# Performance work log

Measured on AMD Instinct MI355X. Metric: run time of the kernel, lower is better.

The kernel has to match this reference:

```python
import jax, jax.numpy as jnp
import numpy as np

D = 192      # d_model
DE = 96      # d_edge
H = 8        # n_heads
DH = D // H  # d_head = 24
DF = 2 * D   # ff hidden = 384
N = 25000
E = 400000


def _layernorm(x, s, b, eps=1e-5):
    m = jnp.mean(x, axis=-1, keepdims=True)
    v = jnp.var(x, axis=-1, keepdims=True)
    return (x - m) * jax.lax.rsqrt(v + eps) * s + b


def setup_inputs() -> dict:
    key = jax.random.key(0)
    ks = jax.random.split(key, 12)
    sc = lambda d: 1.0 / np.sqrt(d)
    inp = {
        "x": jax.random.normal(ks[0], (N, D), jnp.float32),
        "edge_feat": jax.random.normal(ks[1], (E, DE), jnp.float32),
        "edge_index": jax.random.randint(ks[2], (2, E), 0, N, jnp.int64),
        # attention projections (stored [d_in, d_out], applied as x @ W)
        "Wq": jax.random.normal(ks[3], (D, D), jnp.float32) * sc(D),
        "Wk": jax.random.normal(ks[4], (D, D), jnp.float32) * sc(D),
        "Wv": jax.random.normal(ks[5], (D, D), jnp.float32) * sc(D),
        "We": jax.random.normal(ks[6], (DE, H), jnp.float32) * sc(DE),
        "Wo": jax.random.normal(ks[7], (D, D), jnp.float32) * sc(D),
        "bo": jnp.zeros((D,), jnp.float32),
        "Wg": jax.random.normal(ks[8], (2 * D, D), jnp.float32) * sc(2 * D),
        "bg": jnp.zeros((D,), jnp.float32),
        "ln1_s": jnp.ones((D,), jnp.float32),
        "ln1_b": jnp.zeros((D,), jnp.float32),
        "Wf1": jax.random.normal(ks[9], (D, DF), jnp.float32) * sc(D),
        "bf1": jnp.zeros((DF,), jnp.float32),
        "Wf2": jax.random.normal(ks[10], (DF, D), jnp.float32) * sc(DF),
        "bf2": jnp.zeros((D,), jnp.float32),
        "ln2_s": jnp.ones((D,), jnp.float32),
        "ln2_b": jnp.zeros((D,), jnp.float32),
    }
    return inp


def reference(x, edge_feat, edge_index, Wq, Wk, Wv, We, Wo, bo, Wg, bg,
              ln1_s, ln1_b, Wf1, bf1, Wf2, bf2, ln2_s, ln2_b):
    src, dst = edge_index[0], edge_index[1]
    n = x.shape[0]
    # per-edge gathered projections: [E, H, DH]
    q = (x[dst] @ Wq).reshape(-1, H, DH)
    k = (x[src] @ Wk).reshape(-1, H, DH)
    v = (x[src] @ Wv).reshape(-1, H, DH)
    score = jnp.sum(q * k, axis=-1) / np.sqrt(DH) + edge_feat @ We  # [E, H]
    # segment softmax over incoming edges of each dst node
    mx = jax.ops.segment_max(score, dst, num_segments=n)           # [N, H]
    alpha = jnp.exp(score - mx[dst])                                # [E, H]
    den = jax.ops.segment_sum(alpha, dst, num_segments=n)          # [N, H]
    num = jax.ops.segment_sum(alpha[..., None] * v, dst, num_segments=n)  # [N, H, DH]
    agg = (num / (den[:, :, None] + 1e-8)).reshape(n, D)
    o = agg @ Wo + bo
    g = jax.nn.sigmoid(jnp.concatenate([o, x], axis=-1) @ Wg + bg)
    y = _layernorm(g * o + (1.0 - g) * x, ln1_s, ln1_b)
    ff = jax.nn.silu(y @ Wf1 + bf1) @ Wf2 + bf2
    return _layernorm(y + ff, ln2_s, ln2_b)
```

## Files before the change

### kernel.cpp

```cpp
#include <hip/hip_runtime.h>
#include <cstdint>
#include <cstddef>

#define LOG2E 1.4426950408889634f

constexpr int Dm  = 192;
constexpr int DEe = 96;

enum { M_NONE = 0, M_BIAS = 1, M_SILU = 2, M_GATE_LN = 3, M_RES_LN = 4 };

typedef unsigned short u16;
typedef __attribute__((ext_vector_type(8))) short short8v;
typedef __attribute__((ext_vector_type(4))) float f32x4;

__device__ __forceinline__ u16 f2bf(float f) {
    uint32_t u = __builtin_bit_cast(uint32_t, f);
    uint32_t r = (u + 0x7FFF + ((u >> 16) & 1)) >> 16;
    return (u16)r;
}
__device__ __forceinline__ float bf2f(u16 h) {
    uint32_t u = ((uint32_t)h) << 16;
    return __builtin_bit_cast(float, u);
}

__global__ void zero_ints(int* __restrict__ p, int n) {
    int i = blockIdx.x * blockDim.x + threadIdx.x;
    if (i < n) p[i] = 0;
}

__global__ void count_deg(const int* __restrict__ ei, int E, int* __restrict__ deg) {
    int e = blockIdx.x * blockDim.x + threadIdx.x;
    if (e < E) atomicAdd(&deg[ei[E + e]], 1);
}

__global__ __launch_bounds__(1024) void scan_kernel(const int* __restrict__ deg, int N,
                                                    int* __restrict__ offs) {
    __shared__ int sp[1024];
    int t = threadIdx.x;
    int per = (N + 1023) >> 10;
    int base = t * per;
    int sum = 0;
    for (int i = 0; i < per; ++i) {
        int idx = base + i;
        if (idx < N) sum += deg[idx];
    }
    sp[t] = sum;
    __syncthreads();
    for (int off = 1; off < 1024; off <<= 1) {
        int v = (t >= off) ? sp[t - off] : 0;
        __syncthreads();
        sp[t] += v;
        __syncthreads();
    }
    int run = sp[t] - sum;
    for (int i = 0; i < per; ++i) {
        int idx = base + i;
        if (idx < N) { offs[idx] = run; run += deg[idx]; }
    }
    if (t == 1023) offs[N] = sp[1023];
}

__global__ void xconv(const float* __restrict__ x, int n4, u16* __restrict__ xb) {
    int i = blockIdx.x * blockDim.x + threadIdx.x;
    if (i >= n4) return;
    float4 v = ((const float4*)x)[i];
    ushort4 o;
    o.x = f2bf(v.x); o.y = f2bf(v.y); o.z = f2bf(v.z); o.w = f2bf(v.w);
    ((ushort4*)xb)[i] = o;
}

__global__ void prep_w(const float* __restrict__ Wq, const float* __restrict__ Wk,
                       const float* __restrict__ Wv, const float* __restrict__ Wo,
                       const float* __restrict__ Wg, const float* __restrict__ Wf1,
                       const float* __restrict__ Wf2,
                       u16* __restrict__ Wqkvt, u16* __restrict__ Wot,
                       u16* __restrict__ Wgt, u16* __restrict__ Wf1t,
                       u16* __restrict__ Wf2t) {
    int idx = blockIdx.x * blockDim.x + threadIdx.x;
    if (idx < 110592) {
        int n = idx / 192, k = idx % 192;
        const float* W = n < 192 ? Wq : (n < 384 ? Wk : Wv);
        Wqkvt[idx] = f2bf(W[(size_t)k * 192 + (n % 192)]);
    } else if (idx < 147456) {
        int i = idx - 110592;
        int n = i / 192, k = i % 192;
        Wot[i] = f2bf(Wo[(size_t)k * 192 + n]);
    } else if (idx < 221184) {
        int i = idx - 147456;
        int n = i / 384, k = i % 384;
        Wgt[i] = f2bf(Wg[(size_t)k * 192 + n]);
    } else if (idx < 294912) {
        int i = idx - 221184;
        int n = i / 192, k = i % 192;
        Wf1t[i] = f2bf(Wf1[(size_t)k * 384 + n]);
    } else if (idx < 368640) {
        int i = idx - 294912;
        int n = i / 384, k = i % 384;
        Wf2t[i] = f2bf(Wf2[(size_t)k * 192 + n]);
    }
}

__global__ __launch_bounds__(256) void edge_prep(
    const int* __restrict__ ei, int E,
    const float* __restrict__ ef, const float* __restrict__ We,
    const int* __restrict__ offs, int* __restrict__ cur,
    float* __restrict__ scb, int* __restrict__ sbuf)
{
    __shared__ float We_s[DEe * 8];
    __shared__ float ef_s[32][100];
    int tid = threadIdx.x;
    for (int i = tid; i < DEe * 8; i += 256) We_s[i] = We[i];
    int e0 = blockIdx.x * 32;
    #pragma unroll
    for (int rep = 0; rep < 3; ++rep) {
        int idx = tid + 256 * rep;
        int el = idx / 24, c4 = idx % 24;
        int e = e0 + el;
        float4 v = make_float4(0.f, 0.f, 0.f, 0.f);
        if (e < E) v = *(const float4*)&ef[(size_t)e * DEe + c4 * 4];
        *(float4*)&ef_s[el][c4 * 4] = v;
    }
    __syncthreads();
    int el = tid >> 3, h = tid & 7;
    int e = e0 + el;
    if (e >= E) return;
    float epj = 0.f;
    #pragma unroll 8
    for (int i = 0; i < DEe; ++i) epj += ef_s[el][i] * We_s[i * 8 + h];

    int lane = tid & 63;
    int pos = 0;
    if (h == 0) {
        int dst = ei[E + e];
        pos = offs[dst] + atomicAdd(&cur[dst], 1);
    }
    pos = __shfl(pos, lane & 56, 64);
    scb[(size_t)pos * 8 + h] = epj * LOG2E;
    if (h == 0) sbuf[pos] = ei[e];
}

__global__ __launch_bounds__(256) void agg_fused(
    const u16* __restrict__ qkv, const float* __restrict__ scb,
    const int* __restrict__ sbuf, const int* __restrict__ offs,
    int N, u16* __restrict__ aggb)
{
    int node = blockIdx.x * 4 + (threadIdx.x >> 6);
    if (node >= N) return;
    int lane = threadIdx.x & 63;
    int h = lane >> 3;
    int di = (3 * lane) >> 1;
    int odd = lane & 1;

    const uint32_t* qrow = (const uint32_t*)(qkv + (size_t)node * 576);
    uint32_t qd0 = qrow[di], qd1 = qrow[di + 1];
    float q0, q1, q2;
    if (!odd) { q0 = bf2f(qd0 & 0xffff); q1 = bf2f(qd0 >> 16); q2 = bf2f(qd1 & 0xffff); }
    else      { q0 = bf2f(qd0 >> 16);    q1 = bf2f(qd1 & 0xffff); q2 = bf2f(qd1 >> 16); }

    float den = 0.f, a0 = 0.f, a1 = 0.f, a2 = 0.f;
    int beg = offs[node], end = offs[node + 1];

    int src_n = 0; uint32_t kd0_n = 0, kd1_n = 0, vd0_n = 0, vd1_n = 0; float ep_n = 0.f;
    if (beg < end) {
        src_n = sbuf[beg];
        const uint32_t* kr = (const uint32_t*)(qkv + (size_t)src_n * 576 + 192);
        kd0_n = kr[di]; kd1_n = kr[di + 1];
        kd0_n = kd0_n;
        const uint32_t* vr = (const uint32_t*)(qkv + (size_t)src_n * 576 + 384);
        vd0_n = vr[di]; vd1_n = vr[di + 1];
        ep_n = scb[(size_t)beg * 8 + h];
    }

    for (int idx = beg; idx < end; ++idx) {
        uint32_t kd0 = kd0_n, kd1 = kd1_n, vd0 = vd0_n, vd1 = vd1_n;
        float ep = ep_n;
        if (idx + 1 < end) {
            int src = sbuf[idx + 1];
            const uint32_t* kr = (const uint32_t*)(qkv + (size_t)src * 576 + 192);
            kd0_n = kr[di]; kd1_n = kr[di + 1];
            const uint32_t* vr = (const uint32_t*)(qkv + (size_t)src * 576 + 384);
            vd0_n = vr[di]; vd1_n = vr[di + 1];
            ep_n = scb[(size_t)(idx + 1) * 8 + h];
        }
        float k0, k1, k2, v0, v1, v2;
        if (!odd) {
            k0 = bf2f(kd0 & 0xffff); k1 = bf2f(kd0 >> 16); k2 = bf2f(kd1 & 0xffff);
            v0 = bf2f(vd0 & 0xffff); v1 = bf2f(vd0 >> 16); v2 = bf2f(vd1 & 0xffff);
        } else {
            k0 = bf2f(kd0 >> 16); k1 = bf2f(kd1 & 0xffff); k2 = bf2f(kd1 >> 16);
            v0 = bf2f(vd0 >> 16); v1 = bf2f(vd1 & 0xffff); v2 = bf2f(vd1 >> 16);
        }
        float pd = q0 * k0 + q1 * k1 + q2 * k2;
        pd += __shfl_xor(pd, 1, 64);
        pd += __shfl_xor(pd, 2, 64);
        pd += __shfl_xor(pd, 4, 64);
        float p = exp2f(pd * 0.2944885836f + ep);
        den += p;
        a0 += p * v0; a1 += p * v1; a2 += p * v2;
    }
    float rden = 1.f / (den + 1e-8f);
    u16* og = aggb + (size_t)node * Dm;
    int b0 = 3 * lane;
    og[b0]     = f2bf(a0 * rden);
    og[b0 + 1] = f2bf(a1 * rden);
    og[b0 + 2] = f2bf(a2 * rden);
}

__global__ __launch_bounds__(256) void gemm_mfma(
    const u16* __restrict__ A0, const u16* __restrict__ A1, int lda0,
    int M, int K,
    const u16* __restrict__ Wt,
    const float* __restrict__ bias,
    u16* __restrict__ outB, float* __restrict__ outF, int ldo,
    int mode,
    const u16* __restrict__ ep0, const u16* __restrict__ ep1,
    const float* __restrict__ lns, const float* __restrict__ lnb)
{
    __shared__ __align__(16) short As[64 * 72];
    __shared__ __align__(16) short Bs[192 * 72];
    __shared__ float red[2][4][64];

    int tid = threadIdx.x;
    int m0 = blockIdx.x * 64;
    int n0 = blockIdx.y * 192;
    int w = tid >> 6, lane = tid & 63;
    int c16 = lane & 15, hi2 = lane >> 4;

    f32x4 acc[4][3];
    #pragma unroll
    for (int mr = 0; mr < 4; ++mr)
        #pragma unroll
        for (int nr = 0; nr < 3; ++nr) acc[mr][nr] = (f32x4)(0.f);

    int nk = K >> 6;
    short8v ra[2], rb[6];
    auto loadA = [&](int ks) {
        #pragma unroll
        for (int rep = 0; rep < 2; ++rep) {
            int c = tid + 256 * rep;
            int row = c >> 3, kc = c & 7;
            int r = m0 + row; if (r > M - 1) r = M - 1;
            int kg = ks * 64 + kc * 8;
            const u16* base; int ld, kk;
            if (A1 && kg >= 192) { base = A1; ld = 192; kk = kg - 192; }
            else                 { base = A0; ld = lda0; kk = kg; }
            ra[rep] = *(const short8v*)(base + (size_t)r * ld + kk);
        }
    };
    auto loadB = [&](int ks) {
        #pragma unroll
        for (int rep = 0; rep < 6; ++rep) {
            int c = tid + 256 * rep;
            int row = c >> 3, kc = c & 7;
            rb[rep] = *(const short8v*)(Wt + (size_t)(n0 + row) * K + ks * 64 + kc * 8);
        }
    };
    loadA(0); loadB(0);

    for (int ks = 0;;) {
        #pragma unroll
        for (int rep = 0; rep < 2; ++rep) {
            int c = tid + 256 * rep;
            *(short8v*)&As[(c >> 3) * 72 + (c & 7) * 8] = ra[rep];
        }
        #pragma unroll
        for (int rep = 0; rep < 6; ++rep) {
            int c = tid + 256 * rep;
            *(short8v*)&Bs[(c >> 3) * 72 + (c & 7) * 8] = rb[rep];
        }
        __syncthreads();
        ++ks;
        if (ks < nk) { loadA(ks); loadB(ks); }
        #pragma unroll
        for (int kf = 0; kf < 2; ++kf) {
            short8v af[4], bfr[3];
            #pragma unroll
            for (int mr = 0; mr < 4; ++mr)
                af[mr] = *(const short8v*)&As[(mr * 16 + c16) * 72 + kf * 32 + hi2 * 8];
            #pragma unroll
            for (int nr = 0; nr < 3; ++nr)
                bfr[nr] = *(const short8v*)&Bs[(w * 48 + nr * 16 + c16) * 72 + kf * 32 + hi2 * 8];
            #pragma unroll
            for (int mr = 0; mr < 4; ++mr)
                #pragma unroll
                for (int nr = 0; nr < 3; ++nr)
                    acc[mr][nr] = __builtin_amdgcn_mfma_f32_16x16x32_bf16(
                        af[mr], bfr[nr], acc[mr][nr], 0, 0, 0);
        }
        if (ks >= nk) break;
        __syncthreads();
    }

    float bz[3];
    #pragma unroll
    for (int nr = 0; nr < 3; ++nr)
        bz[nr] = bias ? bias[n0 + w * 48 + nr * 16 + c16] : 0.f;

    if (mode <= M_SILU) {
        #pragma unroll
        for (int mr = 0; mr < 4; ++mr)
            #pragma unroll
            for (int reg = 0; reg < 4; ++reg) {
                int r = m0 + mr * 16 + hi2 * 4 + reg;
                if (r >= M) continue;
                #pragma unroll
                for (int nr = 0; nr < 3; ++nr) {
                    float z = acc[mr][nr][reg] + bz[nr];
                    if (mode == M_SILU) z = z / (1.f + expf(-z));
                    int col = n0 + w * 48 + nr * 16 + c16;
                    outB[(size_t)r * ldo + col] = f2bf(z);
                }
            }
        return;
    }

    float s1p[4][4], s2p[4][4];
    #pragma unroll
    for (int mr = 0; mr < 4; ++mr)
        #pragma unroll
        for (int reg = 0; reg < 4; ++reg) {
            int r = m0 + mr * 16 + hi2 * 4 + reg;
            int rc = r < M ? r : M - 1;
            float s1 = 0.f, s2 = 0.f;
            #pragma unroll
            for (int nr = 0; nr < 3; ++nr) {
                int col = w * 48 + nr * 16 + c16;
                float z = acc[mr][nr][reg] + bz[nr];
                float val;
                if (mode == M_GATE_LN) {
                    float g  = 1.f / (1.f + expf(-z));
                    float ov = bf2f(ep0[(size_t)rc * 192 + col]);
                    float xv = bf2f(ep1[(size_t)rc * 192 + col]);
                    val = g * ov + (1.f - g) * xv;
                } else {
                    val = z + bf2f(ep0[(size_t)rc * 192 + col]);
                }
                acc[mr][nr][reg] = val;
                s1 += val; s2 += val * val;
            }
            #pragma unroll
            for (int mS = 1; mS < 16; mS <<= 1) {
                s1 += __shfl_xor(s1, mS, 64);
                s2 += __shfl_xor(s2, mS, 64);
            }
            s1p[mr][reg] = s1; s2p[mr][reg] = s2;
        }
    if (c16 == 0) {
        #pragma unroll
        for (int mr = 0; mr < 4; ++mr)
            #pragma unroll
            for (int reg = 0; reg < 4; ++reg) {
                int rowIdx = mr * 16 + hi2 * 4 + reg;
                red[0][w][rowIdx] = s1p[mr][reg];
                red[1][w][rowIdx] = s2p[mr][reg];
            }
    }
    __syncthreads();
    #pragma unroll
    for (int mr = 0; mr < 4; ++mr)
        #pragma unroll
        for (int reg = 0; reg < 4; ++reg) {
            int rowIdx = mr * 16 + hi2 * 4 + reg;
            int r = m0 + rowIdx;
            if (r >= M) continue;
            float S1 = red[0][0][rowIdx] + red[0][1][rowIdx] + red[0][2][rowIdx] + red[0][3][rowIdx];
            float S2 = red[1][0][rowIdx] + red[1][1][rowIdx] + red[1][2][rowIdx] + red[1][3][rowIdx];
            float mean = S1 * (1.f / 192.f);
            float var  = S2 * (1.f / 192.f) - mean * mean;
            float inv  = rsqrtf(var + 1e-5f);
            #pragma unroll
            for (int nr = 0; nr < 3; ++nr) {
                int col = w * 48 + nr * 16 + c16;
                float res = (acc[mr][nr][reg] - mean) * inv * lns[col] + lnb[col];
                if (mode == M_RES_LN) outF[(size_t)r * 192 + col] = res;
                else                  outB[(size_t)r * 192 + col] = f2bf(res);
            }
        }
}

extern "C" void kernel_launch(void* const* d_in, const int* in_sizes, int n_in,
                              void* d_out, int out_size, void* d_ws, size_t ws_size,
                              hipStream_t stream) {
    const float* x   = (const float*)d_in[0];
    const float* ef  = (const float*)d_in[1];
    const int*   ei  = (const int*)d_in[2];
    const float* Wq  = (const float*)d_in[3];
    const float* Wk  = (const float*)d_in[4];
    const float* Wv  = (const float*)d_in[5];
    const float* We  = (const float*)d_in[6];
    const float* Wo  = (const float*)d_in[7];
    const float* bo  = (const float*)d_in[8];
    const float* Wg  = (const float*)d_in[9];
    const float* bg  = (const float*)d_in[10];
    const float* l1s = (const float*)d_in[11];
    const float* l1b = (const float*)d_in[12];
    const float* Wf1 = (const float*)d_in[13];
    const float* bf1 = (const float*)d_in[14];
    const float* Wf2 = (const float*)d_in[15];
    const float* bf2 = (const float*)d_in[16];
    const float* l2s = (const float*)d_in[17];
    const float* l2b = (const float*)d_in[18];

    int N = in_sizes[0] / Dm;
    int E = in_sizes[1] / DEe;
    float* out = (float*)d_out;

    char* wp = (char*)d_ws;
    auto alloc = [&](size_t bytes) -> void* {
        void* p = wp;
        wp += (bytes + 255) & ~(size_t)255;
        return p;
    };
    size_t NF = (size_t)N * Dm;
    u16*   xb     = (u16*)alloc(NF * 2);
    u16*   qkvb   = (u16*)alloc((size_t)N * 576 * 2);
    u16*   aggb   = (u16*)alloc(NF * 2);
    float* scb    = (float*)alloc((size_t)E * 8 * 4);
    int*   sbuf   = (int*)  alloc((size_t)E * 4);
    int*   degcur = (int*)  alloc((size_t)2 * N * 4);
    int*   offs   = (int*)  alloc((size_t)(N + 1) * 4);
    u16*   Wqkvt  = (u16*)alloc((size_t)576 * 192 * 2);
    u16*   Wot    = (u16*)alloc((size_t)192 * 192 * 2);
    u16*   Wgt    = (u16*)alloc((size_t)192 * 384 * 2);
    u16*   Wf1t   = (u16*)alloc((size_t)384 * 192 * 2);
    u16*   Wf2t   = (u16*)alloc((size_t)192 * 384 * 2);
    u16*   ff1b   = (u16*)alloc((size_t)N * 384 * 2);
    int* deg = degcur;
    int* cur = degcur + N;
    u16* ob = qkvb;
    u16* yb = qkvb + (size_t)N * Dm;

    int gm = (N + 63) / 64;

    prep_w<<<dim3(1440), 256, 0, stream>>>(Wq, Wk, Wv, Wo, Wg, Wf1, Wf2,
        Wqkvt, Wot, Wgt, Wf1t, Wf2t);
    xconv<<<dim3((N * Dm / 4 + 255) / 256), 256, 0, stream>>>(x, N * Dm / 4, xb);
    zero_ints<<<dim3((2 * N + 255) / 256), 256, 0, stream>>>(degcur, 2 * N);
    count_deg<<<dim3((E + 255) / 256), 256, 0, stream>>>(ei, E, deg);
    scan_kernel<<<dim3(1), 1024, 0, stream>>>(deg, N, offs);

    gemm_mfma<<<dim3(gm, 3), 256, 0, stream>>>(xb, nullptr, Dm, N, 192, Wqkvt,
        nullptr, qkvb, nullptr, 576, M_NONE, nullptr, nullptr, nullptr, nullptr);

    edge_prep<<<dim3((E + 31) / 32), 256, 0, stream>>>(ei, E, ef, We,
        offs, cur, scb, sbuf);
    agg_fused<<<dim3((N + 3) / 4), 256, 0, stream>>>(qkvb, scb, sbuf, offs, N, aggb);

    gemm_mfma<<<dim3(gm, 1), 256, 0, stream>>>(aggb, nullptr, Dm, N, 192, Wot,
        bo, ob, nullptr, Dm, M_BIAS, nullptr, nullptr, nullptr, nullptr);

    gemm_mfma<<<dim3(gm, 1), 256, 0, stream>>>(ob, xb, Dm, N, 384, Wgt,
        bg, yb, nullptr, Dm, M_GATE_LN, ob, xb, l1s, l1b);

    gemm_mfma<<<dim3(gm, 2), 256, 0, stream>>>(yb, nullptr, Dm, N, 192, Wf1t,
        bf1, ff1b, nullptr, 384, M_SILU, nullptr, nullptr, nullptr, nullptr);

    gemm_mfma<<<dim3(gm, 1), 256, 0, stream>>>(ff1b, nullptr, 384, N, 384, Wf2t,
        bf2, nullptr, out, Dm, M_RES_LN, yb, nullptr, l2s, l2b);
}
```

Measured before the change: 307.8 us.

## Fuse output projection, gate, LN, and FFN into one per-tile kernel

Replaces four separate GEMM launches (Wo, gate+LN1, FF1+SiLU, FF2+LN2) with a single kernel that keeps each 64-row tile's intermediates in shared memory. This removes the global round trips for o, y and the 384-wide FFN hidden activation, along with three launches. The QKV GEMM and the fused chain now load A and B fragments straight from global memory into registers, with no LDS staging. The risks are higher register and LDS pressure, lower occupancy, and uncoalesced fragment loads of weights that depend on cache hits. The gate now uses the fp32 o accumulator instead of a bf16 round trip, a small precision change.

```diff
diff --git a/kernel.cpp b/kernel.cpp
--- a/kernel.cpp
+++ b/kernel.cpp
@@ -6,8 +6,6 @@
 
 constexpr int Dm  = 192;
 constexpr int DEe = 96;
-
-enum { M_NONE = 0, M_BIAS = 1, M_SILU = 2, M_GATE_LN = 3, M_RES_LN = 4 };
 
 typedef unsigned short u16;
 typedef __attribute__((ext_vector_type(8))) short short8v;
@@ -160,13 +158,12 @@
     float den = 0.f, a0 = 0.f, a1 = 0.f, a2 = 0.f;
     int beg = offs[node], end = offs[node + 1];
 
-    int src_n = 0; uint32_t kd0_n = 0, kd1_n = 0, vd0_n = 0, vd1_n = 0; float ep_n = 0.f;
+    uint32_t kd0_n = 0, kd1_n = 0, vd0_n = 0, vd1_n = 0; float ep_n = 0.f;
     if (beg < end) {
-        src_n = sbuf[beg];
-        const uint32_t* kr = (const uint32_t*)(qkv + (size_t)src_n * 576 + 192);
+        int src = sbuf[beg];
+        const uint32_t* kr = (const uint32_t*)(qkv + (size_t)src * 576 + 192);
         kd0_n = kr[di]; kd1_n = kr[di + 1];
-        kd0_n = kd0_n;
-        const uint32_t* vr = (const uint32_t*)(qkv + (size_t)src_n * 576 + 384);
+        const uint32_t* vr = (const uint32_t*)(qkv + (size_t)src * 576 + 384);
         vd0_n = vr[di]; vd1_n = vr[di + 1];
         ep_n = scb[(size_t)beg * 8 + h];
     }
@@ -206,136 +203,282 @@
     og[b0 + 2] = f2bf(a2 * rden);
 }
 
-__global__ __launch_bounds__(256) void gemm_mfma(
-    const u16* __restrict__ A0, const u16* __restrict__ A1, int lda0,
-    int M, int K,
-    const u16* __restrict__ Wt,
-    const float* __restrict__ bias,
-    u16* __restrict__ outB, float* __restrict__ outF, int ldo,
-    int mode,
-    const u16* __restrict__ ep0, const u16* __restrict__ ep1,
-    const float* __restrict__ lns, const float* __restrict__ lnb)
+__global__ __launch_bounds__(256) void qkv_gemm(
+    const u16* __restrict__ xb, int M,
+    const u16* __restrict__ Wt, u16* __restrict__ qkvb)
 {
-    __shared__ __align__(16) short As[64 * 72];
-    __shared__ __align__(16) short Bs[192 * 72];
+    int tid = threadIdx.x;
+    int m0 = blockIdx.x * 64, n0 = blockIdx.y * 192;
+    int w = tid >> 6, lane = tid & 63;
+    int c16 = lane & 15, hi2 = lane >> 4, kof = hi2 * 8;
+
+    int rcm[4];
+    #pragma unroll
+    for (int mr = 0; mr < 4; ++mr) {
+        int r = m0 + mr * 16 + c16;
+        rcm[mr] = r < M ? r : M - 1;
+    }
+
+    f32x4 acc[4][3];
+    #pragma unroll
+    for (int mr = 0; mr < 4; ++mr)
+        #pragma unroll
+        for (int nr = 0; nr < 3; ++nr) acc[mr][nr] = (f32x4)(0.f);
+
+    #pragma unroll
+    for (int ks = 0; ks < 6; ++ks) {
+        short8v af[4], bfr[3];
+        #pragma unroll
+        for (int mr = 0; mr < 4; ++mr)
+            af[mr] = *(const short8v*)(xb + (size_t)rcm[mr] * 192 + ks * 32 + kof);
+        #pragma unroll
+        for (int nr = 0; nr < 3; ++nr)
+            bfr[nr] = *(const short8v*)(Wt + (size_t)(n0 + w * 48 + nr * 16 + c16) * 192 + ks * 32 + kof);
+        #pragma unroll
+        for (int mr = 0; mr < 4; ++mr)
+            #pragma unroll
+            for (int nr = 0; nr < 3; ++nr)
+                acc[mr][nr] = __builtin_amdgcn_mfma_f32_16x16x32_bf16(
+                    af[mr], bfr[nr], acc[mr][nr], 0, 0, 0);
+    }
+
+    #pragma unroll
+    for (int mr = 0; mr < 4; ++mr)
+        #pragma unroll
+        for (int reg = 0; reg < 4; ++reg) {
+            int r = m0 + mr * 16 + hi2 * 4 + reg;
+            if (r >= M) continue;
+            #pragma unroll
+            for (int nr = 0; nr < 3; ++nr)
+                qkvb[(size_t)r * 576 + n0 + w * 48 + nr * 16 + c16] =
+                    f2bf(acc[mr][nr][reg]);
+        }
+}
+
+__global__ __launch_bounds__(256) void chain_fused(
+    const u16* __restrict__ aggb, const u16* __restrict__ xb, int M,
+    const u16* __restrict__ Wot, const float* __restrict__ bo,
+    const u16* __restrict__ Wgt, const float* __restrict__ bg,
+    const float* __restrict__ l1s, const float* __restrict__ l1b,
+    const u16* __restrict__ Wf1t, const float* __restrict__ bf1,
+    const u16* __restrict__ Wf2t, const float* __restrict__ bf2,
+    const float* __restrict__ l2s, const float* __restrict__ l2b,
+    float* __restrict__ out)
+{
+    __shared__ __align__(16) short Ybuf[64 * 200];
+    __shared__ __align__(16) short Fbuf[64 * 392];
     __shared__ float red[2][4][64];
 
     int tid = threadIdx.x;
     int m0 = blockIdx.x * 64;
-    int n0 = blockIdx.y * 192;
     int w = tid >> 6, lane = tid & 63;
-    int c16 = lane & 15, hi2 = lane >> 4;
-
-    f32x4 acc[4][3];
-    #pragma unroll
-    for (int mr = 0; mr < 4; ++mr)
-        #pragma unroll
-        for (int nr = 0; nr < 3; ++nr) acc[mr][nr] = (f32x4)(0.f);
-
-    int nk = K >> 6;
-    short8v ra[2], rb[6];
-    auto loadA = [&](int ks) {
-        #pragma unroll
-        for (int rep = 0; rep < 2; ++rep) {
-            int c = tid + 256 * rep;
-            int row = c >> 3, kc = c & 7;
-            int r = m0 + row; if (r > M - 1) r = M - 1;
-            int kg = ks * 64 + kc * 8;
-            const u16* base; int ld, kk;
-            if (A1 && kg >= 192) { base = A1; ld = 192; kk = kg - 192; }
-            else                 { base = A0; ld = lda0; kk = kg; }
-            ra[rep] = *(const short8v*)(base + (size_t)r * ld + kk);
-        }
-    };
-    auto loadB = [&](int ks) {
-        #pragma unroll
-        for (int rep = 0; rep < 6; ++rep) {
-            int c = tid + 256 * rep;
-            int row = c >> 3, kc = c & 7;
-            rb[rep] = *(const short8v*)(Wt + (size_t)(n0 + row) * K + ks * 64 + kc * 8);
-        }
-    };
-    loadA(0); loadB(0);
-
-    for (int ks = 0;;) {
-        #pragma unroll
-        for (int rep = 0; rep < 2; ++rep) {
-            int c = tid + 256 * rep;
-            *(short8v*)&As[(c >> 3) * 72 + (c & 7) * 8] = ra[rep];
-        }
-        #pragma unroll
-        for (int rep = 0; rep < 6; ++rep) {
-            int c = tid + 256 * rep;
-            *(short8v*)&Bs[(c >> 3) * 72 + (c & 7) * 8] = rb[rep];
-        }
-        __syncthreads();
-        ++ks;
-        if (ks < nk) { loadA(ks); loadB(ks); }
-        #pragma unroll
-        for (int kf = 0; kf < 2; ++kf) {
-            short8v af[4], bfr[3];
-            #pragma unroll
-            for (int mr = 0; mr < 4; ++mr)
-                af[mr] = *(const short8v*)&As[(mr * 16 + c16) * 72 + kf * 32 + hi2 * 8];
+    int c16 = lane & 15, hi2 = lane >> 4, kof = hi2 * 8;
+
+    int rcm[4];
+    #pragma unroll
+    for (int mr = 0; mr < 4; ++mr) {
+        int r = m0 + mr * 16 + c16;
+        rcm[mr] = r < M ? r : M - 1;
+    }
+
+    f32x4 oacc[4][3];
+    #pragma unroll
+    for (int mr = 0; mr < 4; ++mr)
+        #pragma unroll
+        for (int nr = 0; nr < 3; ++nr) oacc[mr][nr] = (f32x4)(0.f);
+    #pragma unroll
+    for (int ks = 0; ks < 6; ++ks) {
+        short8v af[4], bfr[3];
+        #pragma unroll
+        for (int mr = 0; mr < 4; ++mr)
+            af[mr] = *(const short8v*)(aggb + (size_t)rcm[mr] * 192 + ks * 32 + kof);
+        #pragma unroll
+        for (int nr = 0; nr < 3; ++nr)
+            bfr[nr] = *(const short8v*)(Wot + (size_t)(w * 48 + nr * 16 + c16) * 192 + ks * 32 + kof);
+        #pragma unroll
+        for (int mr = 0; mr < 4; ++mr)
             #pragma unroll
             for (int nr = 0; nr < 3; ++nr)
-                bfr[nr] = *(const short8v*)&Bs[(w * 48 + nr * 16 + c16) * 72 + kf * 32 + hi2 * 8];
-            #pragma unroll
-            for (int mr = 0; mr < 4; ++mr)
-                #pragma unroll
-                for (int nr = 0; nr < 3; ++nr)
-                    acc[mr][nr] = __builtin_amdgcn_mfma_f32_16x16x32_bf16(
-                        af[mr], bfr[nr], acc[mr][nr], 0, 0, 0);
-        }
-        if (ks >= nk) break;
-        __syncthreads();
-    }
-
-    float bz[3];
-    #pragma unroll
-    for (int nr = 0; nr < 3; ++nr)
-        bz[nr] = bias ? bias[n0 + w * 48 + nr * 16 + c16] : 0.f;
-
-    if (mode <= M_SILU) {
+                oacc[mr][nr] = __builtin_amdgcn_mfma_f32_16x16x32_bf16(
+                    af[mr], bfr[nr], oacc[mr][nr], 0, 0, 0);
+    }
+    #pragma unroll
+    for (int nr = 0; nr < 3; ++nr) {
+        int col = w * 48 + nr * 16 + c16;
+        float b = bo[col];
         #pragma unroll
         for (int mr = 0; mr < 4; ++mr)
             #pragma unroll
             for (int reg = 0; reg < 4; ++reg) {
-                int r = m0 + mr * 16 + hi2 * 4 + reg;
-                if (r >= M) continue;
-                #pragma unroll
-                for (int nr = 0; nr < 3; ++nr) {
-                    float z = acc[mr][nr][reg] + bz[nr];
-                    if (mode == M_SILU) z = z / (1.f + expf(-z));
-                    int col = n0 + w * 48 + nr * 16 + c16;
-                    outB[(size_t)r * ldo + col] = f2bf(z);
-                }
-            }
-        return;
-    }
-
+                oacc[mr][nr][reg] += b;
+                int row = mr * 16 + hi2 * 4 + reg;
+                Ybuf[row * 200 + col] = (short)f2bf(oacc[mr][nr][reg]);
+            }
+    }
+    __syncthreads();
+
+    f32x4 zacc[4][3];
+    #pragma unroll
+    for (int mr = 0; mr < 4; ++mr)
+        #pragma unroll
+        for (int nr = 0; nr < 3; ++nr) zacc[mr][nr] = (f32x4)(0.f);
+    #pragma unroll
+    for (int ks = 0; ks < 6; ++ks) {
+        short8v af[4], bfr[3];
+        #pragma unroll
+        for (int mr = 0; mr < 4; ++mr)
+            af[mr] = *(const short8v*)&Ybuf[(mr * 16 + c16) * 200 + ks * 32 + kof];
+        #pragma unroll
+        for (int nr = 0; nr < 3; ++nr)
+            bfr[nr] = *(const short8v*)(Wgt + (size_t)(w * 48 + nr * 16 + c16) * 384 + ks * 32 + kof);
+        #pragma unroll
+        for (int mr = 0; mr < 4; ++mr)
+            #pragma unroll
+            for (int nr = 0; nr < 3; ++nr)
+                zacc[mr][nr] = __builtin_amdgcn_mfma_f32_16x16x32_bf16(
+                    af[mr], bfr[nr], zacc[mr][nr], 0, 0, 0);
+    }
+    #pragma unroll
+    for (int ks = 6; ks < 12; ++ks) {
+        short8v af[4], bfr[3];
+        #pragma unroll
+        for (int mr = 0; mr < 4; ++mr)
+            af[mr] = *(const short8v*)(xb + (size_t)rcm[mr] * 192 + (ks - 6) * 32 + kof);
+        #pragma unroll
+        for (int nr = 0; nr < 3; ++nr)
+            bfr[nr] = *(const short8v*)(Wgt + (size_t)(w * 48 + nr * 16 + c16) * 384 + ks * 32 + kof);
+        #pragma unroll
+        for (int mr = 0; mr < 4; ++mr)
+            #pragma unroll
+            for (int nr = 0; nr < 3; ++nr)
+                zacc[mr][nr] = __builtin_amdgcn_mfma_f32_16x16x32_bf16(
+                    af[mr], bfr[nr], zacc[mr][nr], 0, 0, 0);
+    }
     float s1p[4][4], s2p[4][4];
     #pragma unroll
     for (int mr = 0; mr < 4; ++mr)
         #pragma unroll
         for (int reg = 0; reg < 4; ++reg) {
-            int r = m0 + mr * 16 + hi2 * 4 + reg;
-            int rc = r < M ? r : M - 1;
+            int gr = m0 + mr * 16 + hi2 * 4 + reg;
+            int rcR = gr < M ? gr : M - 1;
             float s1 = 0.f, s2 = 0.f;
             #pragma unroll
             for (int nr = 0; nr < 3; ++nr) {
                 int col = w * 48 + nr * 16 + c16;
-                float z = acc[mr][nr][reg] + bz[nr];
-                float val;
-                if (mode == M_GATE_LN) {
-                    float g  = 1.f / (1.f + expf(-z));
-                    float ov = bf2f(ep0[(size_t)rc * 192 + col]);
-                    float xv = bf2f(ep1[(size_t)rc * 192 + col]);
-                    val = g * ov + (1.f - g) * xv;
-                } else {
-                    val = z + bf2f(ep0[(size_t)rc * 192 + col]);
-                }
-                acc[mr][nr][reg] = val;
+                float z = zacc[mr][nr][reg] + bg[col];
+                float g = 1.f / (1.f + expf(-z));
+                float xv = bf2f(xb[(size_t)rcR * 192 + col]);
+                float val = g * oacc[mr][nr][reg] + (1.f - g) * xv;
+                zacc[mr][nr][reg] = val;
+                s1 += val; s2 += val * val;
+            }
+            #pragma unroll
+            for (int mS = 1; mS < 16; mS <<= 1) {
+                s1 += __shfl_xor(s1, mS, 64);
+                s2 += __shfl_xor(s2, mS, 64);
+            }
+            s1p[mr][reg] = s1; s2p[mr][reg] = s2;
+        }
+    if (c16 == 0) {
+        #pragma unroll
+        for (int mr = 0; mr < 4; ++mr)
+            #pragma unroll
+            for (int reg = 0; reg < 4; ++reg) {
+                int rowIdx = mr * 16 + hi2 * 4 + reg;
+                red[0][w][rowIdx] = s1p[mr][reg];
+                red[1][w][rowIdx] = s2p[mr][reg];
+            }
+    }
+    __syncthreads();
+    #pragma unroll
+    for (int mr = 0; mr < 4; ++mr)
+        #pragma unroll
+        for (int reg = 0; reg < 4; ++reg) {
+            int rowIdx = mr * 16 + hi2 * 4 + reg;
+            float S1 = red[0][0][rowIdx] + red[0][1][rowIdx] + red[0][2][rowIdx] + red[0][3][rowIdx];
+            float S2 = red[1][0][rowIdx] + red[1][1][rowIdx] + red[1][2][rowIdx] + red[1][3][rowIdx];
+            float mean = S1 * (1.f / 192.f);
+            float var  = S2 * (1.f / 192.f) - mean * mean;
+            float inv  = rsqrtf(var + 1e-5f);
+            #pragma unroll
+            for (int nr = 0; nr < 3; ++nr) {
+                int col = w * 48 + nr * 16 + c16;
+                float yv = (zacc[mr][nr][reg] - mean) * inv * l1s[col] + l1b[col];
+                zacc[mr][nr][reg] = yv;
+                Ybuf[rowIdx * 200 + col] = (short)f2bf(yv);
+            }
+        }
+    __syncthreads();
+
+    f32x4 tacc[4][6];
+    #pragma unroll
+    for (int mr = 0; mr < 4; ++mr)
+        #pragma unroll
+        for (int nr = 0; nr < 6; ++nr) tacc[mr][nr] = (f32x4)(0.f);
+    #pragma unroll
+    for (int ks = 0; ks < 6; ++ks) {
+        short8v af[4], bfr[6];
+        #pragma unroll
+        for (int mr = 0; mr < 4; ++mr)
+            af[mr] = *(const short8v*)&Ybuf[(mr * 16 + c16) * 200 + ks * 32 + kof];
+        #pragma unroll
+        for (int nr = 0; nr < 6; ++nr)
+            bfr[nr] = *(const short8v*)(Wf1t + (size_t)(w * 96 + nr * 16 + c16) * 192 + ks * 32 + kof);
+        #pragma unroll
+        for (int mr = 0; mr < 4; ++mr)
+            #pragma unroll
+            for (int nr = 0; nr < 6; ++nr)
+                tacc[mr][nr] = __builtin_amdgcn_mfma_f32_16x16x32_bf16(
+                    af[mr], bfr[nr], tacc[mr][nr], 0, 0, 0);
+    }
+    #pragma unroll
+    for (int nr = 0; nr < 6; ++nr) {
+        int col = w * 96 + nr * 16 + c16;
+        float b = bf1[col];
+        #pragma unroll
+        for (int mr = 0; mr < 4; ++mr)
+            #pragma unroll
+            for (int reg = 0; reg < 4; ++reg) {
+                float z = tacc[mr][nr][reg] + b;
+                float t = z / (1.f + expf(-z));
+                int row = mr * 16 + hi2 * 4 + reg;
+                Fbuf[row * 392 + col] = (short)f2bf(t);
+            }
+    }
+    __syncthreads();
+
+    f32x4 facc[4][3];
+    #pragma unroll
+    for (int mr = 0; mr < 4; ++mr)
+        #pragma unroll
+        for (int nr = 0; nr < 3; ++nr) facc[mr][nr] = (f32x4)(0.f);
+    #pragma unroll
+    for (int ks = 0; ks < 12; ++ks) {
+        short8v af[4], bfr[3];
+        #pragma unroll
+        for (int mr = 0; mr < 4; ++mr)
+            af[mr] = *(const short8v*)&Fbuf[(mr * 16 + c16) * 392 + ks * 32 + kof];
+        #pragma unroll
+        for (int nr = 0; nr < 3; ++nr)
+            bfr[nr] = *(const short8v*)(Wf2t + (size_t)(w * 48 + nr * 16 + c16) * 384 + ks * 32 + kof);
+        #pragma unroll
+        for (int mr = 0; mr < 4; ++mr)
+            #pragma unroll
+            for (int nr = 0; nr < 3; ++nr)
+                facc[mr][nr] = __builtin_amdgcn_mfma_f32_16x16x32_bf16(
+                    af[mr], bfr[nr], facc[mr][nr], 0, 0, 0);
+    }
+    #pragma unroll
+    for (int mr = 0; mr < 4; ++mr)
+        #pragma unroll
+        for (int reg = 0; reg < 4; ++reg) {
+            int rowIdx = mr * 16 + hi2 * 4 + reg;
+            float s1 = 0.f, s2 = 0.f;
+            #pragma unroll
+            for (int nr = 0; nr < 3; ++nr) {
+                int col = w * 48 + nr * 16 + c16;
+                float val = facc[mr][nr][reg] + bf2[col] + bf2f((u16)Ybuf[rowIdx * 200 + col]);
+                facc[mr][nr][reg] = val;
                 s1 += val; s2 += val * val;
             }
             #pragma unroll
@@ -371,9 +514,8 @@
             #pragma unroll
             for (int nr = 0; nr < 3; ++nr) {
                 int col = w * 48 + nr * 16 + c16;
-                float res = (acc[mr][nr][reg] - mean) * inv * lns[col] + lnb[col];
-                if (mode == M_RES_LN) outF[(size_t)r * 192 + col] = res;
-                else                  outB[(size_t)r * 192 + col] = f2bf(res);
+                out[(size_t)r * 192 + col] =
+                    (facc[mr][nr][reg] - mean) * inv * l2s[col] + l2b[col];
             }
         }
 }
@@ -424,11 +566,8 @@
     u16*   Wgt    = (u16*)alloc((size_t)192 * 384 * 2);
     u16*   Wf1t   = (u16*)alloc((size_t)384 * 192 * 2);
     u16*   Wf2t   = (u16*)alloc((size_t)192 * 384 * 2);
-    u16*   ff1b   = (u16*)alloc((size_t)N * 384 * 2);
     int* deg = degcur;
     int* cur = degcur + N;
-    u16* ob = qkvb;
-    u16* yb = qkvb + (size_t)N * Dm;
 
     int gm = (N + 63) / 64;
 
@@ -439,22 +578,12 @@
     count_deg<<<dim3((E + 255) / 256), 256, 0, stream>>>(ei, E, deg);
     scan_kernel<<<dim3(1), 1024, 0, stream>>>(deg, N, offs);
 
-    gemm_mfma<<<dim3(gm, 3), 256, 0, stream>>>(xb, nullptr, Dm, N, 192, Wqkvt,
-        nullptr, qkvb, nullptr, 576, M_NONE, nullptr, nullptr, nullptr, nullptr);
+    qkv_gemm<<<dim3(gm, 3), 256, 0, stream>>>(xb, N, Wqkvt, qkvb);
 
     edge_prep<<<dim3((E + 31) / 32), 256, 0, stream>>>(ei, E, ef, We,
         offs, cur, scb, sbuf);
     agg_fused<<<dim3((N + 3) / 4), 256, 0, stream>>>(qkvb, scb, sbuf, offs, N, aggb);
 
-    gemm_mfma<<<dim3(gm, 1), 256, 0, stream>>>(aggb, nullptr, Dm, N, 192, Wot,
-        bo, ob, nullptr, Dm, M_BIAS, nullptr, nullptr, nullptr, nullptr);
-
-    gemm_mfma<<<dim3(gm, 1), 256, 0, stream>>>(ob, xb, Dm, N, 384, Wgt,
-        bg, yb, nullptr, Dm, M_GATE_LN, ob, xb, l1s, l1b);
-
-    gemm_mfma<<<dim3(gm, 2), 256, 0, stream>>>(yb, nullptr, Dm, N, 192, Wf1t,
-        bf1, ff1b, nullptr, 384, M_SILU, nullptr, nullptr, nullptr, nullptr);
-
-    gemm_mfma<<<dim3(gm, 1), 256, 0, stream>>>(ff1b, nullptr, 384, N, 384, Wf2t,
-        bf2, nullptr, out, Dm, M_RES_LN, yb, nullptr, l2s, l2b);
-}
+    chain_fused<<<dim3(gm), 256, 0, stream>>>(aggb, xb, N,
+        Wot, bo, Wgt, bg, l1s, l1b, Wf1t, bf1, Wf2t, bf2, l2s, l2b, out);
+}
```

New measurement: 295.2 us. 1.04x faster.
